# Kernel optimization log

Measured on AMD Instinct MI355X. Metric: run time of the kernel, lower is better.

## Reference

```python
import jax, jax.numpy as jnp
import numpy as np

EMBED_DIM = 1024
NUM_HEADS = 16
D_K = EMBED_DIM // NUM_HEADS


def setup_inputs() -> dict:
    key = jax.random.key(0)
    ks = jax.random.split(key, 5)
    s = 1.0 / np.sqrt(EMBED_DIM)  # roughly match nn.Linear init scale
    return {
        "x": jax.random.normal(ks[0], (2, 2048, EMBED_DIM), dtype=jnp.float32),
        "wq": jax.random.normal(ks[1], (EMBED_DIM, EMBED_DIM), dtype=jnp.float32) * s,
        "wk": jax.random.normal(ks[2], (EMBED_DIM, EMBED_DIM), dtype=jnp.float32) * s,
        "wv": jax.random.normal(ks[3], (EMBED_DIM, EMBED_DIM), dtype=jnp.float32) * s,
        "wo": jax.random.normal(ks[4], (EMBED_DIM, EMBED_DIM), dtype=jnp.float32) * s,
    }


def reference(x, wq, wk, wv, wo):
    b, s, e = x.shape
    # nn.Linear(bias=False): y = x @ W.T
    def split_heads(t):
        return t.reshape(b, s, NUM_HEADS, D_K).transpose(0, 2, 1, 3)  # [b,h,s,d]
    q = split_heads(x @ wq.T)
    k = split_heads(x @ wk.T)
    v = split_heads(x @ wv.T)
    scores = jnp.einsum("bhqd,bhkd->bhqk", q, k) / jnp.sqrt(jnp.float32(D_K))
    attn = jax.nn.softmax(scores, axis=-1)
    out = jnp.einsum("bhqk,bhkd->bhqd", attn, v)  # [b,h,s,d]
    out = out.transpose(0, 2, 1, 3).reshape(b, s, e)
    return out @ wo.T
```

## Files before the change

kernel.cpp:

```cpp
#include <hip/hip_runtime.h>
#include <stdint.h>

typedef unsigned short u16;
typedef float f32x4 __attribute__((ext_vector_type(4)));
typedef __bf16 bf16x8 __attribute__((ext_vector_type(8)));

__device__ __forceinline__ u16 f2bf(float f) {
  union { float f; uint32_t u; } c; c.f = f;
  uint32_t u = c.u;
  u += 0x7fffu + ((u >> 16) & 1u);
  return (u16)(u >> 16);
}

__device__ __forceinline__ uint32_t pkbf(float a, float b) {
  union { float f; uint32_t u; } ua, ub; ua.f = a; ub.f = b;
  return __builtin_amdgcn_perm(ub.u, ua.u, 0x07060302u);
}

#define GLOAD_LDS16(g, l)                                                              \
  __builtin_amdgcn_global_load_lds((__attribute__((address_space(1))) void*)(g),       \
                                   (__attribute__((address_space(3))) void*)(l), 16, 0, 0)

__global__ __launch_bounds__(256) void cvt_all(const float* __restrict__ x,
                                               const float* __restrict__ wq,
                                               const float* __restrict__ wk,
                                               const float* __restrict__ wv,
                                               const float* __restrict__ wo,
                                               u16* __restrict__ xb,
                                               u16* __restrict__ wqkvb,
                                               u16* __restrict__ wob) {
  int bx = blockIdx.x;
  const float* src;
  u16* dst;
  int i;
  if (bx < 4096) {
    src = x; dst = xb; i = bx * 256 + threadIdx.x;
  } else {
    int r = bx - 4096;
    int w = r >> 10;
    i = (r & 1023) * 256 + threadIdx.x;
    if (w == 0)      { src = wq; dst = wqkvb; }
    else if (w == 1) { src = wk; dst = wqkvb + 1048576; }
    else if (w == 2) { src = wv; dst = wqkvb + 2097152; }
    else             { src = wo; dst = wob; }
  }
  const float4 v = ((const float4*)src)[i];
  ushort4 o;
  o.x = f2bf(v.x); o.y = f2bf(v.y); o.z = f2bf(v.z); o.w = f2bf(v.w);
  ((ushort4*)dst)[i] = o;
}

__global__ __launch_bounds__(256) void gemm_qkv(const u16* __restrict__ A,
                                                const u16* __restrict__ B,
                                                u16* __restrict__ QKb,
                                                u16* __restrict__ Vt) {
  const int K = 1024;
  __shared__ __align__(16) u16 sA[128 * 32];
  __shared__ __align__(16) u16 sB[128 * 32];
  const int tid = threadIdx.x;
  const int lane = tid & 63;
  const int wave = tid >> 6;
  const int quad = lane >> 4, l16 = lane & 15;
  const int wm = (wave >> 1) * 64, wn = (wave & 1) * 64;
  const int bm = blockIdx.y * 128, bn = blockIdx.x * 128;

  const int ar = tid >> 2;
  const int ac = (tid & 3) * 8;

  f32x4 acc[4][4];
#pragma unroll
  for (int i = 0; i < 4; i++)
#pragma unroll
    for (int j = 0; j < 4; j++) acc[i][j] = (f32x4){0.f, 0.f, 0.f, 0.f};

  const u16* pA0 = A + (size_t)(bm + ar) * K + ac;
  const u16* pA1 = A + (size_t)(bm + 64 + ar) * K + ac;
  const u16* pB0 = B + (size_t)(bn + ar) * K + ac;
  const u16* pB1 = B + (size_t)(bn + 64 + ar) * K + ac;

  for (int k0 = 0; k0 < K; k0 += 32) {
    GLOAD_LDS16(pA0 + k0, (char*)sA + tid * 16);
    GLOAD_LDS16(pA1 + k0, (char*)sA + 4096 + tid * 16);
    GLOAD_LDS16(pB0 + k0, (char*)sB + tid * 16);
    GLOAD_LDS16(pB1 + k0, (char*)sB + 4096 + tid * 16);
    __syncthreads();
    bf16x8 af[4], bfr[4];
#pragma unroll
    for (int mt = 0; mt < 4; mt++)
      af[mt] = *(const bf16x8*)&sA[(wm + mt * 16 + l16) * 32 + quad * 8];
#pragma unroll
    for (int nt = 0; nt < 4; nt++)
      bfr[nt] = *(const bf16x8*)&sB[(wn + nt * 16 + l16) * 32 + quad * 8];
#pragma unroll
    for (int mt = 0; mt < 4; mt++)
#pragma unroll
      for (int nt = 0; nt < 4; nt++)
        acc[mt][nt] = __builtin_amdgcn_mfma_f32_16x16x32_bf16(af[mt], bfr[nt], acc[mt][nt], 0, 0, 0);
    __syncthreads();
  }

  if (blockIdx.x < 16) {
    const float qs = (blockIdx.x < 8) ? 0.125f : 1.0f;
#pragma unroll
    for (int mt = 0; mt < 4; mt++)
#pragma unroll
      for (int nt = 0; nt < 4; nt++)
#pragma unroll
        for (int r = 0; r < 4; r++) {
          int row = bm + wm + mt * 16 + quad * 4 + r;
          int col = bn + wn + nt * 16 + l16;
          QKb[(size_t)row * 2048 + col] = f2bf(acc[mt][nt][r] * qs);
        }
  } else {
#pragma unroll
    for (int mt = 0; mt < 4; mt++)
#pragma unroll
      for (int nt = 0; nt < 4; nt++) {
        int hd = (bn - 2048) + wn + nt * 16 + l16;
        int tok = bm + wm + mt * 16 + quad * 4;
        ushort4 o;
        o.x = f2bf(acc[mt][nt][0]);
        o.y = f2bf(acc[mt][nt][1]);
        o.z = f2bf(acc[mt][nt][2]);
        o.w = f2bf(acc[mt][nt][3]);
        *(ushort4*)&Vt[(size_t)hd * 4096 + tok] = o;
      }
  }
}

__global__ __launch_bounds__(256, 3) void attn_fwd(const u16* __restrict__ QKb,
                                                   const u16* __restrict__ Vt,
                                                   u16* __restrict__ O) {
  const int bx = blockIdx.x;
  const int qt = bx >> 5;
  const int h  = (bx >> 1) & 15;
  const int b  = bx & 1;
  const int tid = threadIdx.x;
  const int lane = tid & 63;
  const int wave = tid >> 6;
  const int quad = lane >> 4, l16 = lane & 15;

  __shared__ __align__(16) u16 smem[24576];
  u16* sK0 = smem;
  u16* sK1 = smem + 4096;
  u16* sV0 = smem + 8192;
  u16* sV1 = smem + 12288;
  u16* sQ  = smem + 16384;

  const int tok0 = b * 2048;
  const int q0 = qt * 128;
  const int colh = h * 64;

#pragma unroll
  for (int k2 = 0; k2 < 4; k2++) {
    int c = k2 * 256 + tid;
    int row = c >> 3, c8 = (c & 7) ^ (row & 7);
    GLOAD_LDS16(QKb + (size_t)(tok0 + q0 + row) * 2048 + colh + c8 * 8,
                (char*)sQ + c * 16);
  }
#pragma unroll
  for (int k2 = 0; k2 < 2; k2++) {
    int c = k2 * 256 + tid;
    int row = c >> 3, c8 = (c & 7) ^ (row & 7);
    GLOAD_LDS16(QKb + (size_t)(tok0 + row) * 2048 + 1024 + colh + c8 * 8,
                (char*)sK0 + c * 16);
    GLOAD_LDS16(Vt + (size_t)(colh + row) * 4096 + tok0 + c8 * 8,
                (char*)sV0 + c * 16);
  }
  __syncthreads();

  bf16x8 aq[2][2];
#pragma unroll
  for (int sub = 0; sub < 2; sub++)
#pragma unroll
    for (int kh = 0; kh < 2; kh++) {
      int row = wave * 32 + sub * 16 + l16;
      aq[sub][kh] = *(const bf16x8*)&sQ[row * 64 + (((kh * 4 + quad) ^ (row & 7)) * 8)];
    }

  f32x4 oacc[2][4];
  float lsum[2] = {0.f, 0.f};
#pragma unroll
  for (int sub = 0; sub < 2; sub++)
#pragma unroll
    for (int nt = 0; nt < 4; nt++) oacc[sub][nt] = (f32x4){0.f, 0.f, 0.f, 0.f};

  const int srcA = ((quad & 1) * 32 + l16);
  const int srcB = srcA + 16;
  const bool hiT = (quad >= 2);

  int p = 0;
  for (int it = 0; it < 32; ++it) {
    u16* sKc = p ? sK1 : sK0;
    u16* sVc = p ? sV1 : sV0;
    if (it < 31) {
      u16* sKn = p ? sK0 : sK1;
      u16* sVn = p ? sV0 : sV1;
      const int nkv = (it + 1) * 64;
#pragma unroll
      for (int k2 = 0; k2 < 2; k2++) {
        int c = k2 * 256 + tid;
        int row = c >> 3, c8 = (c & 7) ^ (row & 7);
        GLOAD_LDS16(QKb + (size_t)(tok0 + nkv + row) * 2048 + 1024 + colh + c8 * 8,
                    (char*)sKn + c * 16);
        GLOAD_LDS16(Vt + (size_t)(colh + row) * 4096 + tok0 + nkv + c8 * 8,
                    (char*)sVn + c * 16);
      }
    }

    bf16x8 kf[4][2], vf[4][2];
#pragma unroll
    for (int nt = 0; nt < 4; nt++)
#pragma unroll
      for (int kh = 0; kh < 2; kh++) {
        int rr = nt * 16 + l16;
        int off = rr * 64 + (((kh * 4 + quad) ^ (rr & 7)) * 8);
        kf[nt][kh] = *(const bf16x8*)&sKc[off];
        vf[nt][kh] = *(const bf16x8*)&sVc[off];
      }

#pragma unroll
    for (int sub = 0; sub < 2; sub++) {
      f32x4 e[4];
#pragma unroll
      for (int nt = 0; nt < 4; nt++) {
        f32x4 c = (f32x4){0.f, 0.f, 0.f, 0.f};
        c = __builtin_amdgcn_mfma_f32_16x16x32_bf16(kf[nt][0], aq[sub][0], c, 0, 0, 0);
        c = __builtin_amdgcn_mfma_f32_16x16x32_bf16(kf[nt][1], aq[sub][1], c, 0, 0, 0);
#pragma unroll
        for (int r = 0; r < 4; r++) e[nt][r] = __expf(c[r]);
        lsum[sub] += (e[nt][0] + e[nt][1]) + (e[nt][2] + e[nt][3]);
      }
#pragma unroll
      for (int kh = 0; kh < 2; kh++) {
        uint32_t pk0 = pkbf(e[2 * kh][0], e[2 * kh][1]);
        uint32_t pk1 = pkbf(e[2 * kh][2], e[2 * kh][3]);
        uint32_t pk2_ = pkbf(e[2 * kh + 1][0], e[2 * kh + 1][1]);
        uint32_t pk3_ = pkbf(e[2 * kh + 1][2], e[2 * kh + 1][3]);
        uint32_t a0 = (uint32_t)__shfl((int)pk0, srcA, 64);
        uint32_t c0 = (uint32_t)__shfl((int)pk2_, srcA, 64);
        uint32_t a1 = (uint32_t)__shfl((int)pk1, srcA, 64);
        uint32_t c1 = (uint32_t)__shfl((int)pk3_, srcA, 64);
        uint32_t a2 = (uint32_t)__shfl((int)pk0, srcB, 64);
        uint32_t c2 = (uint32_t)__shfl((int)pk2_, srcB, 64);
        uint32_t a3 = (uint32_t)__shfl((int)pk1, srcB, 64);
        uint32_t c3 = (uint32_t)__shfl((int)pk3_, srcB, 64);
        union { uint32_t u[4]; bf16x8 v; } bb;
        bb.u[0] = hiT ? c0 : a0;
        bb.u[1] = hiT ? c1 : a1;
        bb.u[2] = hiT ? c2 : a2;
        bb.u[3] = hiT ? c3 : a3;
#pragma unroll
        for (int nt = 0; nt < 4; nt++)
          oacc[sub][nt] = __builtin_amdgcn_mfma_f32_16x16x32_bf16(vf[nt][kh], bb.v, oacc[sub][nt], 0, 0, 0);
      }
    }
    __syncthreads();
    p ^= 1;
  }

#pragma unroll
  for (int sub = 0; sub < 2; sub++) {
    float v = lsum[sub];
    v += __shfl_xor(v, 16, 64);
    v += __shfl_xor(v, 32, 64);
    lsum[sub] = 1.0f / v;
  }

  u16* sT = smem + wave * 6144;
#pragma unroll
  for (int sub = 0; sub < 2; sub++)
#pragma unroll
    for (int nt = 0; nt < 4; nt++)
#pragma unroll
      for (int r = 0; r < 4; r++)
        sT[(sub * 16 + l16) * 68 + nt * 16 + quad * 4 + r] = f2bf(oacc[sub][nt][r] * lsum[sub]);
#pragma unroll
  for (int k = 0; k < 4; k++) {
    int qrow = k * 8 + (lane >> 3);
    int cch = lane & 7;
    uint4 vrow = *(const uint4*)&sT[qrow * 68 + cch * 8];
    int tokr = tok0 + q0 + wave * 32 + qrow;
    *(uint4*)&O[(size_t)tokr * 1024 + colh + cch * 8] = vrow;
  }
}

__global__ __launch_bounds__(256) void gemm_out(const u16* __restrict__ A,
                                                const u16* __restrict__ B,
                                                float* __restrict__ C) {
  const int N = 1024, K = 1024;
  __shared__ __align__(16) u16 sA[128 * 32];
  __shared__ __align__(16) u16 sB[64 * 32];
  const int tid = threadIdx.x;
  const int lane = tid & 63;
  const int wave = tid >> 6;
  const int quad = lane >> 4, l16 = lane & 15;
  const int wm = (wave >> 1) * 64, wn = (wave & 1) * 32;
  const int bm = blockIdx.y * 128, bn = blockIdx.x * 64;
  const int ar = tid >> 2;
  const int ac = (tid & 3) * 8;

  f32x4 acc[4][2];
#pragma unroll
  for (int i = 0; i < 4; i++)
#pragma unroll
    for (int j = 0; j < 2; j++) acc[i][j] = (f32x4){0.f, 0.f, 0.f, 0.f};

  const u16* pA0 = A + (size_t)(bm + ar) * K + ac;
  const u16* pA1 = A + (size_t)(bm + 64 + ar) * K + ac;
  const u16* pB0 = B + (size_t)(bn + ar) * K + ac;

  for (int k0 = 0; k0 < K; k0 += 32) {
    GLOAD_LDS16(pA0 + k0, (char*)sA + tid * 16);
    GLOAD_LDS16(pA1 + k0, (char*)sA + 4096 + tid * 16);
    GLOAD_LDS16(pB0 + k0, (char*)sB + tid * 16);
    __syncthreads();
    bf16x8 af[4], bfr[2];
#pragma unroll
    for (int mt = 0; mt < 4; mt++)
      af[mt] = *(const bf16x8*)&sA[(wm + mt * 16 + l16) * 32 + quad * 8];
#pragma unroll
    for (int nt = 0; nt < 2; nt++)
      bfr[nt] = *(const bf16x8*)&sB[(wn + nt * 16 + l16) * 32 + quad * 8];
#pragma unroll
    for (int mt = 0; mt < 4; mt++)
#pragma unroll
      for (int nt = 0; nt < 2; nt++)
        acc[mt][nt] = __builtin_amdgcn_mfma_f32_16x16x32_bf16(af[mt], bfr[nt], acc[mt][nt], 0, 0, 0);
    __syncthreads();
  }

#pragma unroll
  for (int mt = 0; mt < 4; mt++)
#pragma unroll
    for (int nt = 0; nt < 2; nt++)
#pragma unroll
      for (int r = 0; r < 4; r++) {
        int row = bm + wm + mt * 16 + quad * 4 + r;
        int col = bn + wn + nt * 16 + l16;
        C[(size_t)row * N + col] = acc[mt][nt][r];
      }
}

extern "C" void kernel_launch(void* const* d_in, const int* in_sizes, int n_in,
                              void* d_out, int out_size, void* d_ws, size_t ws_size,
                              hipStream_t stream) {
  const float* x  = (const float*)d_in[0];
  const float* wq = (const float*)d_in[1];
  const float* wk = (const float*)d_in[2];
  const float* wv = (const float*)d_in[3];
  const float* wo = (const float*)d_in[4];
  float* out = (float*)d_out;
  char* ws = (char*)d_ws;
  const size_t MB = 1u << 20;

  u16* xb    = (u16*)(ws);
  u16* wqkvb = (u16*)(ws + 8 * MB);
  u16* wob   = (u16*)(ws + 14 * MB);
  u16* QKb   = (u16*)(ws + 16 * MB);
  u16* Vtb   = (u16*)(ws + 32 * MB);
  u16* Ob    = xb;

  cvt_all<<<8192, 256, 0, stream>>>(x, wq, wk, wv, wo, xb, wqkvb, wob);

  gemm_qkv<<<dim3(24, 32), 256, 0, stream>>>(xb, wqkvb, QKb, Vtb);

  attn_fwd<<<512, 256, 0, stream>>>(QKb, Vtb, Ob);

  gemm_out<<<dim3(16, 32), 256, 0, stream>>>(Ob, wob, out);
}
```

Measured before the change: 204.9 us.

## Use 16x16x16 MFMA for PV to drop shuffles, fold log2e into Q scale

The PV product now uses the 16x16x16 bf16 MFMA, so the exponentiated scores from the QK MFMA output can be packed straight into the B operand. This removes the eight cross-lane shuffles and selects per step, and V fragments are reloaded from LDS in 4-element pieces to match. The Q scale now also folds in log2(e), so the cheaper native exp2 replaces __expf. The trade is twice as many smaller MFMA instructions and more LDS reads of V, with the same total math.

Result: faster. 194.8 us (-4.9%).

```diff
diff --git a/kernel.cpp b/kernel.cpp
--- a/kernel.cpp
+++ b/kernel.cpp
@@ -4,6 +4,7 @@
 typedef unsigned short u16;
 typedef float f32x4 __attribute__((ext_vector_type(4)));
 typedef __bf16 bf16x8 __attribute__((ext_vector_type(8)));
+typedef short s16x4 __attribute__((ext_vector_type(4)));
 
 __device__ __forceinline__ u16 f2bf(float f) {
   union { float f; uint32_t u; } c; c.f = f;
@@ -100,7 +101,7 @@
   }
 
   if (blockIdx.x < 16) {
-    const float qs = (blockIdx.x < 8) ? 0.125f : 1.0f;
+    const float qs = (blockIdx.x < 8) ? 0.18033688011f : 1.0f;
 #pragma unroll
     for (int mt = 0; mt < 4; mt++)
 #pragma unroll
@@ -183,11 +184,7 @@
 #pragma unroll
   for (int sub = 0; sub < 2; sub++)
 #pragma unroll
-    for (int nt = 0; nt < 4; nt++) oacc[sub][nt] = (f32x4){0.f, 0.f, 0.f, 0.f};
-
-  const int srcA = ((quad & 1) * 32 + l16);
-  const int srcB = srcA + 16;
-  const bool hiT = (quad >= 2);
+    for (int db = 0; db < 4; db++) oacc[sub][db] = (f32x4){0.f, 0.f, 0.f, 0.f};
 
   int p = 0;
   for (int it = 0; it < 32; ++it) {
@@ -208,51 +205,44 @@
       }
     }
 
-    bf16x8 kf[4][2], vf[4][2];
+    bf16x8 kf[4][2];
 #pragma unroll
     for (int nt = 0; nt < 4; nt++)
 #pragma unroll
       for (int kh = 0; kh < 2; kh++) {
         int rr = nt * 16 + l16;
-        int off = rr * 64 + (((kh * 4 + quad) ^ (rr & 7)) * 8);
-        kf[nt][kh] = *(const bf16x8*)&sKc[off];
-        vf[nt][kh] = *(const bf16x8*)&sVc[off];
+        kf[nt][kh] = *(const bf16x8*)&sKc[rr * 64 + (((kh * 4 + quad) ^ (rr & 7)) * 8)];
+      }
+    s16x4 vf[4][4];
+#pragma unroll
+    for (int db = 0; db < 4; db++)
+#pragma unroll
+      for (int nt = 0; nt < 4; nt++) {
+        int row = db * 16 + l16;
+        int c16 = (nt * 2 + (quad >> 1)) ^ (row & 7);
+        vf[db][nt] = *(const s16x4*)&sVc[row * 64 + c16 * 8 + (quad & 1) * 4];
       }
 
 #pragma unroll
     for (int sub = 0; sub < 2; sub++) {
-      f32x4 e[4];
+      float e[4][4];
 #pragma unroll
       for (int nt = 0; nt < 4; nt++) {
         f32x4 c = (f32x4){0.f, 0.f, 0.f, 0.f};
         c = __builtin_amdgcn_mfma_f32_16x16x32_bf16(kf[nt][0], aq[sub][0], c, 0, 0, 0);
         c = __builtin_amdgcn_mfma_f32_16x16x32_bf16(kf[nt][1], aq[sub][1], c, 0, 0, 0);
 #pragma unroll
-        for (int r = 0; r < 4; r++) e[nt][r] = __expf(c[r]);
+        for (int r = 0; r < 4; r++) e[nt][r] = __builtin_amdgcn_exp2f(c[r]);
         lsum[sub] += (e[nt][0] + e[nt][1]) + (e[nt][2] + e[nt][3]);
       }
 #pragma unroll
-      for (int kh = 0; kh < 2; kh++) {
-        uint32_t pk0 = pkbf(e[2 * kh][0], e[2 * kh][1]);
-        uint32_t pk1 = pkbf(e[2 * kh][2], e[2 * kh][3]);
-        uint32_t pk2_ = pkbf(e[2 * kh + 1][0], e[2 * kh + 1][1]);
-        uint32_t pk3_ = pkbf(e[2 * kh + 1][2], e[2 * kh + 1][3]);
-        uint32_t a0 = (uint32_t)__shfl((int)pk0, srcA, 64);
-        uint32_t c0 = (uint32_t)__shfl((int)pk2_, srcA, 64);
-        uint32_t a1 = (uint32_t)__shfl((int)pk1, srcA, 64);
-        uint32_t c1 = (uint32_t)__shfl((int)pk3_, srcA, 64);
-        uint32_t a2 = (uint32_t)__shfl((int)pk0, srcB, 64);
-        uint32_t c2 = (uint32_t)__shfl((int)pk2_, srcB, 64);
-        uint32_t a3 = (uint32_t)__shfl((int)pk1, srcB, 64);
-        uint32_t c3 = (uint32_t)__shfl((int)pk3_, srcB, 64);
-        union { uint32_t u[4]; bf16x8 v; } bb;
-        bb.u[0] = hiT ? c0 : a0;
-        bb.u[1] = hiT ? c1 : a1;
-        bb.u[2] = hiT ? c2 : a2;
-        bb.u[3] = hiT ? c3 : a3;
-#pragma unroll
-        for (int nt = 0; nt < 4; nt++)
-          oacc[sub][nt] = __builtin_amdgcn_mfma_f32_16x16x32_bf16(vf[nt][kh], bb.v, oacc[sub][nt], 0, 0, 0);
+      for (int nt = 0; nt < 4; nt++) {
+        union { uint32_t u[2]; s16x4 v; } bb;
+        bb.u[0] = pkbf(e[nt][0], e[nt][1]);
+        bb.u[1] = pkbf(e[nt][2], e[nt][3]);
+#pragma unroll
+        for (int db = 0; db < 4; db++)
+          oacc[sub][db] = __builtin_amdgcn_mfma_f32_16x16x16bf16_1k(vf[db][nt], bb.v, oacc[sub][db], 0, 0, 0);
       }
     }
     __syncthreads();
@@ -271,10 +261,10 @@
 #pragma unroll
   for (int sub = 0; sub < 2; sub++)
 #pragma unroll
-    for (int nt = 0; nt < 4; nt++)
+    for (int db = 0; db < 4; db++)
 #pragma unroll
       for (int r = 0; r < 4; r++)
-        sT[(sub * 16 + l16) * 68 + nt * 16 + quad * 4 + r] = f2bf(oacc[sub][nt][r] * lsum[sub]);
+        sT[(sub * 16 + l16) * 68 + db * 16 + quad * 4 + r] = f2bf(oacc[sub][db][r] * lsum[sub]);
 #pragma unroll
   for (int k = 0; k < 4; k++) {
     int qrow = k * 8 + (lane >> 3);
```
